# Optimization experiments

Measured on AMD Instinct MI355X. Metric: run time of the kernel, lower is better.

Reference implementation:

```python
import jax, jax.numpy as jnp
import numpy as np

B, C_IN, T, H, W = 4, 512, 4, 56, 56
G, GP, K = 8, 64, 56            # groups, group_planes, kernel_size (H == K)
OUT = G * GP                     # out_channels = 512
EPS = 1e-5


def setup_inputs() -> dict:
    key = jax.random.key(0)
    ks = jax.random.split(key, 9)
    x = jax.random.normal(ks[0], (B, C_IN, T, H, W), jnp.float32)
    w_qkv = jax.random.normal(ks[1], (2 * OUT, C_IN), jnp.float32) * np.sqrt(1.0 / C_IN)
    g_qkv = jax.random.uniform(ks[2], (2 * OUT,), jnp.float32, 0.5, 1.5)
    b_qkv = jax.random.normal(ks[3], (2 * OUT,), jnp.float32) * 0.1
    relative = jax.random.normal(ks[4], (2 * GP, 2 * K - 1), jnp.float32) * np.sqrt(1.0 / GP)
    g_sim = jax.random.uniform(ks[5], (3 * G,), jnp.float32, 0.5, 1.5)
    b_sim = jax.random.normal(ks[6], (3 * G,), jnp.float32) * 0.1
    g_out = jax.random.uniform(ks[7], (2 * OUT,), jnp.float32, 0.5, 1.5)
    b_out = jax.random.normal(ks[8], (2 * OUT,), jnp.float32) * 0.1
    return {"x": x, "w_qkv": w_qkv, "g_qkv": g_qkv, "b_qkv": b_qkv,
            "relative": relative, "g_sim": g_sim, "b_sim": b_sim,
            "g_out": g_out, "b_out": b_out}


def _bn(x, gamma, beta, axes):
    # training-mode batchnorm: batch stats over `axes`, per channel (dim 1)
    mean = jnp.mean(x, axes, keepdims=True)
    var = jnp.var(x, axes, keepdims=True)
    shp = [1] * x.ndim
    shp[1] = -1
    return gamma.reshape(shp) * (x - mean) * jax.lax.rsqrt(var + EPS) + beta.reshape(shp)


def reference(x, w_qkv, g_qkv, b_qkv, relative, g_sim, b_sim, g_out, b_out):
    # axial='height': (B,C,T,H,W) -> (B,T,W,C,H), attend along H
    xp = jnp.transpose(x, (0, 2, 4, 1, 3)).reshape(B * T * W, C_IN, H)
    # 1x1 Conv1d + BatchNorm1d
    qkv = _bn(jnp.einsum('oc,nch->noh', w_qkv, xp), g_qkv, b_qkv, (0, 2))
    qkv = qkv.reshape(-1, G, 2 * GP, H)
    q, k, v = qkv[:, :, :GP // 2], qkv[:, :, GP // 2:GP], qkv[:, :, GP:]
    qk = jnp.einsum('bgci,bgcj->bgij', q, k)
    # relative position embeddings gathered per (i, j) offset
    idx = jnp.arange(K)[:, None] - jnp.arange(K)[None, :] + K - 1  # (K, K)
    emb = relative[:, idx]                                         # (2*GP, K, K)
    q_e, k_e, v_e = emb[:GP // 2], emb[GP // 2:GP], emb[GP:]
    qr = jnp.einsum('bgci,cij->bgij', q, q_e)
    kr = jnp.swapaxes(jnp.einsum('bgci,cij->bgij', k, k_e), 2, 3)
    sim = _bn(jnp.concatenate([qk, qr, kr], axis=1), g_sim, b_sim, (0, 2, 3))
    sim = sim.reshape(-1, 3, G, H, H).sum(axis=1)
    sim = jax.nn.softmax(sim, axis=3)
    sv = jnp.einsum('bgij,bgcj->bgci', sim, v)
    sve = jnp.einsum('bgij,cij->bgci', sim, v_e)
    out = jnp.concatenate([sv, sve], axis=-1).reshape(-1, 2 * OUT, H)
    out = _bn(out, g_out, b_out, (0, 2))
    out = out.reshape(B, T, W, OUT, 2, H).sum(axis=-2)
    return jnp.transpose(out, (0, 3, 1, 4, 2))  # (B, OUT, T, H, W)
```

## Files before the change

### kernel.cpp

```cpp
#include <hip/hip_runtime.h>
#include <hip/hip_bf16.h>

#define EPS 1e-5f
typedef __hip_bfloat16 bf;
typedef __attribute__((ext_vector_type(8))) short bf16x8;
typedef __attribute__((ext_vector_type(4))) short s16x4;
typedef __attribute__((ext_vector_type(4))) float f32x4;

#define MFMA16(a, b, c) __builtin_amdgcn_mfma_f32_16x16x32_bf16(a, b, c, 0, 0, 0)

#define WS_QSUM     0
#define WS_QSQ      4096
#define WS_SIMSUM   8192
#define WS_SIMSQ    9728
#define WS_OUTSUM   11264
#define WS_OUTSQ    19456
#define WS_ZERO_END 27648
#define WS_AQKV     27648
#define WS_BQKV     28672
#define WS_ASIM     29696
#define WS_BSIM     29728
#define WS_AOUT     29760
#define WS_BOUT     30784

__device__ __forceinline__ void gload_lds16(const void* g, void* l) {
    __builtin_amdgcn_global_load_lds(
        (const __attribute__((address_space(1))) void*)g,
        (__attribute__((address_space(3))) void*)l, 16, 0, 0);
}
__device__ __forceinline__ float bfbits2f(short b) {
    return __uint_as_float(((uint32_t)(unsigned short)b) << 16);
}
__device__ __forceinline__ short f2bfbits(float f) {
    return (short)__hip_bfloat16_raw(__float2bfloat16(f)).x;
}

__global__ __launch_bounds__(256) void k0_transpose(const float* __restrict__ x,
                                                    bf* __restrict__ xbt) {
    int bid = blockIdx.x;
    int h = bid % 56, bt = bid / 56;
    int b = bt >> 2, t = bt & 3;
    __shared__ short tile[512 * 57];
    const float* src = x + (((size_t)(b * 512) * 4 + t) * 3136) + h * 56;
    for (int e = threadIdx.x; e < 512 * 56; e += 256) {
        int c = e / 56, w = e - c * 56;
        tile[c * 57 + w] = f2bfbits(src[(size_t)c * 12544 + w]);
    }
    __syncthreads();
    short* dst = reinterpret_cast<short*>(xbt);
    size_t pbase = ((size_t)bt * 56) * 56 + h;
    for (int e = threadIdx.x; e < 512 * 56; e += 256) {
        int w = e >> 9, c = e & 511;
        dst[(pbase + (size_t)w * 56) * 512 + c] = tile[c * 57 + w];
    }
}

__global__ __launch_bounds__(256) void kw_conv(const float* __restrict__ w, bf* __restrict__ wb) {
    int i = (blockIdx.x * 256 + threadIdx.x) * 4;
#pragma unroll
    for (int u = 0; u < 4; ++u) wb[i + u] = __float2bfloat16(w[i + u]);
}

__global__ __launch_bounds__(256) void kprep(const float* __restrict__ rel,
                                             short* __restrict__ relTq,
                                             short* __restrict__ relTk,
                                             short* __restrict__ relBv) {
    int tid = blockIdx.x * 256 + threadIdx.x;
    if (tid < 3584) {
        int d = tid >> 5, c = tid & 31;
        relTq[tid] = f2bfbits(d < 111 ? rel[c * 111 + d] : 0.f);
        relTk[tid] = f2bfbits(d < 111 ? rel[(32 + c) * 111 + d] : 0.f);
    } else if (tid < 11776) {
        int u = tid - 3584, c = u >> 7, d = u & 127;
        relBv[u] = f2bfbits(d < 111 ? rel[(64 + c) * 111 + d] : 0.f);
    }
}

__global__ __launch_bounds__(256) void k1_mfma(const bf* __restrict__ xbt,
                                               const bf* __restrict__ wb,
                                               short* __restrict__ qkP,
                                               short* __restrict__ vP,
                                               float* __restrict__ qsum,
                                               float* __restrict__ qsq) {
    __shared__ __align__(16) short As[8192];
    __shared__ __align__(16) short Bs[7168];
    int tid = threadIdx.x;
    int g  = blockIdx.x;
    int p0 = blockIdx.y * 112;
    int o0 = g * 128;
    const short* aG = reinterpret_cast<const short*>(wb);
    const short* bG = reinterpret_cast<const short*>(xbt);
    int wv = tid >> 6, l = tid & 63, r16 = l & 15, q4 = l >> 4;

    f32x4 acc[2][7];
#pragma unroll
    for (int i = 0; i < 2; ++i)
#pragma unroll
        for (int j = 0; j < 7; ++j) acc[i][j] = (f32x4){0.f, 0.f, 0.f, 0.f};

    int rowa0 = wv * 32 + r16, rowa1 = rowa0 + 16;

    for (int k0 = 0; k0 < 512; k0 += 64) {
        int ch = tid;
#pragma unroll
        for (int it = 0; it < 4; ++it, ch += 256) {
            int row = ch >> 3, c = ch & 7;
            int gc = (c ^ row) & 7;
            gload_lds16(aG + (((size_t)(o0 + row)) << 9) + k0 + gc * 8, &As[ch << 3]);
        }
        ch = tid;
#pragma unroll
        for (int it = 0; it < 3; ++it, ch += 256) {
            int row = ch >> 3, c = ch & 7;
            int gc = (c ^ row) & 7;
            gload_lds16(bG + (((size_t)(p0 + row)) << 9) + k0 + gc * 8, &Bs[ch << 3]);
        }
        if (tid < 128) {
            int u = tid + 768;
            int row = u >> 3, c = u & 7;
            int gc = (c ^ row) & 7;
            gload_lds16(bG + (((size_t)(p0 + row)) << 9) + k0 + gc * 8, &Bs[u << 3]);
        }
        __syncthreads();
#pragma unroll
        for (int kk = 0; kk < 2; ++kk) {
            int wch = kk * 4 + q4;
            bf16x8 a0 = *reinterpret_cast<const bf16x8*>(&As[rowa0 * 64 + ((wch ^ rowa0) & 7) * 8]);
            bf16x8 a1 = *reinterpret_cast<const bf16x8*>(&As[rowa1 * 64 + ((wch ^ rowa1) & 7) * 8]);
#pragma unroll
            for (int j = 0; j < 7; ++j) {
                int rowb = j * 16 + r16;
                bf16x8 bj = *reinterpret_cast<const bf16x8*>(&Bs[rowb * 64 + ((wch ^ rowb) & 7) * 8]);
                acc[0][j] = MFMA16(a0, bj, acc[0][j]);
                acc[1][j] = MFMA16(a1, bj, acc[1][j]);
            }
        }
        __syncthreads();
    }
    int bkt = blockIdx.y & 3;
#pragma unroll
    for (int i = 0; i < 2; ++i)
#pragma unroll
        for (int r = 0; r < 4; ++r) {
            float sA = 0.f, sB = 0.f;
#pragma unroll
            for (int j = 0; j < 7; ++j) { float v = acc[i][j][r]; sA += v; sB += v * v; }
#pragma unroll
            for (int mk = 1; mk < 16; mk <<= 1) { sA += __shfl_xor(sA, mk); sB += __shfl_xor(sB, mk); }
            if (r16 == 0) {
                int o = o0 + wv * 32 + i * 16 + q4 * 4 + r;
                atomicAdd(&qsum[o * 4 + bkt], sA);
                atomicAdd(&qsq [o * 4 + bkt], sB);
            }
        }
#pragma unroll
    for (int j = 0; j < 7; ++j) {
        int p = p0 + j * 16 + r16;
        size_t rowb = ((size_t)g * 50176 + p) * 64;
#pragma unroll
        for (int i = 0; i < 2; ++i) {
            int op = wv * 32 + i * 16 + q4 * 4;
            s16x4 pk;
#pragma unroll
            for (int r = 0; r < 4; ++r) pk[r] = f2bfbits(acc[i][j][r]);
            short* dst = (op < 64) ? (qkP + rowb + op) : (vP + rowb + (op - 64));
            *reinterpret_cast<s16x4*>(dst) = pk;
        }
    }
}

__global__ __launch_bounds__(256) void k1b_coef(const float* __restrict__ qsum, const float* __restrict__ qsq,
                                                const float* __restrict__ gamma, const float* __restrict__ beta,
                                                float* __restrict__ a_c, float* __restrict__ b_c) {
    int o = blockIdx.x * 256 + threadIdx.x;
    float s = qsum[o * 4] + qsum[o * 4 + 1] + qsum[o * 4 + 2] + qsum[o * 4 + 3];
    float s2 = qsq[o * 4] + qsq[o * 4 + 1] + qsq[o * 4 + 2] + qsq[o * 4 + 3];
    float inv = 1.f / 50176.f;
    float mean = s * inv;
    float var = s2 * inv - mean * mean;
    float a = gamma[o] * rsqrtf(var + EPS);
    a_c[o] = a; b_c[o] = beta[o] - a * mean;
}

__global__ __launch_bounds__(512) void kbn2(const short* __restrict__ qkP,
                                            short* __restrict__ vP,
                                            const float* __restrict__ aq, const float* __restrict__ bq,
                                            const short* __restrict__ relTq,
                                            const short* __restrict__ relTk,
                                            float* __restrict__ ssum, float* __restrict__ ssq) {
    __shared__ __align__(16) short qkTl[5120];
    __shared__ short vtl[64 * 57];
    __shared__ float red[48];
    int blk = blockIdx.x, n = blk >> 3, g = blk & 7, tid = threadIdx.x;
    size_t sb = ((size_t)g * 50176 + (size_t)n * 56) * 64;
    const short* qsrc = qkP + sb;
    short* vsrc = vP + sb;
    for (int u = tid; u < 448; u += 512) {
        int i = u >> 3, c0 = (u & 7) << 3;
        bf16x8 raw = *reinterpret_cast<const bf16x8*>(qsrc + i * 64 + c0);
        bf16x8 t;
#pragma unroll
        for (int uu = 0; uu < 8; ++uu) {
            int o = g * 128 + c0 + uu;
            t[uu] = f2bfbits(aq[o] * bfbits2f(raw[uu]) + bq[o]);
        }
        *reinterpret_cast<bf16x8*>(&qkTl[((c0 & 32) ? 2560 : 0) + i * 40 + (c0 & 31)]) = t;
    }
    for (int u = tid; u < 640; u += 512) {
        int part = u / 320, r = u - part * 320;
        qkTl[part * 2560 + (56 + r / 40) * 40 + (r % 40)] = 0;
    }
    for (int u = tid; u < 448; u += 512) {
        int i = u >> 3, c0 = (u & 7) << 3;
        bf16x8 raw = *reinterpret_cast<const bf16x8*>(vsrc + i * 64 + c0);
#pragma unroll
        for (int uu = 0; uu < 8; ++uu) {
            int o = g * 128 + 64 + c0 + uu;
            vtl[(c0 + uu) * 57 + i] = f2bfbits(aq[o] * bfbits2f(raw[uu]) + bq[o]);
        }
    }
    __syncthreads();
    for (int u = tid; u < 448; u += 512) {
        int c = u / 7, h0 = (u - c * 7) * 8;
        bf16x8 t;
#pragma unroll
        for (int uu = 0; uu < 8; ++uu) t[uu] = vtl[c * 57 + h0 + uu];
        *reinterpret_cast<bf16x8*>(vsrc + c * 56 + h0) = t;
    }
    int w = tid >> 6, l = tid & 63, m = w >> 1, s = w & 1, la = l & 15, lb = l >> 4;
    bf16x8 aqf = *reinterpret_cast<const bf16x8*>(&qkTl[(m * 16 + la) * 40 + lb * 8]);
    bf16x8 akf = *reinterpret_cast<const bf16x8*>(&qkTl[2560 + (m * 16 + la) * 40 + lb * 8]);
    float s0 = 0, s1 = 0, s2v = 0, q0 = 0, q1 = 0, q2 = 0;
#pragma unroll
    for (int t = 0; t < 2; ++t) {
        int nt = 2 * s + t;
        bf16x8 bk = *reinterpret_cast<const bf16x8*>(&qkTl[2560 + (nt * 16 + la) * 40 + lb * 8]);
        f32x4 acc = {0, 0, 0, 0};
        acc = MFMA16(aqf, bk, acc);
        int j = nt * 16 + la;
        if (j < 56) {
#pragma unroll
            for (int r = 0; r < 4; ++r) {
                int i = m * 16 + lb * 4 + r;
                if (i < 56) { float v = acc[r]; s0 += v; q0 += v * v; }
            }
        }
    }
    int ndt = s ? 3 : 4, dt0 = s * 4;
    for (int t = 0; t < ndt; ++t) {
        int dt = dt0 + t;
        bf16x8 br = *reinterpret_cast<const bf16x8*>(relTq + (dt * 16 + la) * 32 + lb * 8);
        f32x4 acc = {0, 0, 0, 0};
        acc = MFMA16(aqf, br, acc);
        int d = dt * 16 + la;
#pragma unroll
        for (int r = 0; r < 4; ++r) {
            int i = m * 16 + lb * 4 + r;
            if (i < 56 && d >= i && d <= i + 55) { float v = acc[r]; s1 += v; q1 += v * v; }
        }
    }
    for (int t = 0; t < ndt; ++t) {
        int dt = dt0 + t;
        bf16x8 br = *reinterpret_cast<const bf16x8*>(relTk + (dt * 16 + la) * 32 + lb * 8);
        f32x4 acc = {0, 0, 0, 0};
        acc = MFMA16(akf, br, acc);
        int d = dt * 16 + la;
#pragma unroll
        for (int r = 0; r < 4; ++r) {
            int j = m * 16 + lb * 4 + r;
            if (j < 56 && d >= j && d <= j + 55) { float v = acc[r]; s2v += v; q2 += v * v; }
        }
    }
    float vals[6] = {s0, s1, s2v, q0, q1, q2};
#pragma unroll
    for (int v = 0; v < 6; ++v) {
        for (int off = 32; off; off >>= 1) vals[v] += __shfl_down(vals[v], off);
        if (l == 0) red[v * 8 + w] = vals[v];
    }
    __syncthreads();
    if (tid < 6) {
        float tot = 0;
#pragma unroll
        for (int k = 0; k < 8; ++k) tot += red[tid * 8 + k];
        int comp = (tid < 3) ? tid : tid - 3;
        int ch = comp * 8 + g;
        int bkt = blk & 63;
        atomicAdd((tid < 3 ? ssum : ssq) + ch * 64 + bkt, tot);
    }
}

__global__ void k2b_coef(const float* __restrict__ ssum, const float* __restrict__ ssq,
                         const float* __restrict__ gs, const float* __restrict__ bs,
                         float* __restrict__ a_c, float* __restrict__ b_c) {
    int c = threadIdx.x;
    if (c >= 24) return;
    float s = 0, s2 = 0;
    for (int k = 0; k < 64; ++k) { s += ssum[c * 64 + k]; s2 += ssq[c * 64 + k]; }
    float inv = 1.f / 2809856.f;
    float mean = s * inv;
    float var = s2 * inv - mean * mean;
    float a = gs[c] * rsqrtf(var + EPS);
    a_c[c] = a; b_c[c] = bs[c] - a * mean;
}

__global__ __launch_bounds__(512, 6) void k3_mfma(const short* __restrict__ relTq,
                                                  const short* __restrict__ relTk,
                                                  const short* __restrict__ relBv,
                                                  short* __restrict__ qkP,
                                                  short* __restrict__ vP,
                                                  const float* __restrict__ aq, const float* __restrict__ bq,
                                                  const float* __restrict__ asim, const float* __restrict__ bsim,
                                                  float* __restrict__ osum, float* __restrict__ osq) {
    __shared__ __align__(16) char smem[51936];
    short* qkTl = (short*)smem;
    float* qkl  = (float*)(smem + 10240);
    short* Sql  = (short*)(smem + 23008);
    short* Krl  = (short*)(smem + 36448);
    short* simB = (short*)(smem + 23008);
    short* Pb   = (short*)(smem + 32224);
    short* vBl  = (short*)smem;
    float* red  = (float*)(smem + 49888);

    int blk = blockIdx.x, n = blk >> 3, g = blk & 7, tid = threadIdx.x;
    size_t sb = ((size_t)g * 50176 + (size_t)n * 56) * 64;
    short* svdst = qkP + sb;
    short* vHs   = vP + sb;

    bf16x8 vreg = {0, 0, 0, 0, 0, 0, 0, 0};
    int vc = tid / 7, vch = tid - vc * 7;
    if (tid < 448)
        vreg = *reinterpret_cast<const bf16x8*>(vHs + vc * 56 + vch * 8);

    for (int u = tid; u < 448; u += 512) {
        int i = u >> 3, c0 = (u & 7) << 3;
        bf16x8 raw = *reinterpret_cast<const bf16x8*>(svdst + i * 64 + c0);
        bf16x8 t;
#pragma unroll
        for (int uu = 0; uu < 8; ++uu) {
            int o = g * 128 + c0 + uu;
            t[uu] = f2bfbits(aq[o] * bfbits2f(raw[uu]) + bq[o]);
        }
        *reinterpret_cast<bf16x8*>(&qkTl[((c0 & 32) ? 2560 : 0) + i * 40 + (c0 & 31)]) = t;
    }
    for (int u = tid; u < 640; u += 512) {
        int part = u / 320, r = u - part * 320;
        qkTl[part * 2560 + (56 + r / 40) * 40 + (r % 40)] = 0;
    }
    __syncthreads();

    int w = tid >> 6, l = tid & 63, m = w >> 1, s = w & 1, la = l & 15, lb = l >> 4;
    int i0 = m * 16 + lb * 4;
    {
        bf16x8 aqf = *reinterpret_cast<const bf16x8*>(&qkTl[(m * 16 + la) * 40 + lb * 8]);
        bf16x8 akf = *reinterpret_cast<const bf16x8*>(&qkTl[(64 + m * 16 + la) * 40 + lb * 8]);
        __builtin_amdgcn_s_setprio(1);
#pragma unroll
        for (int t = 0; t < 2; ++t) {
            int nt = 2 * s + t;
            bf16x8 bk = *reinterpret_cast<const bf16x8*>(&qkTl[(64 + nt * 16 + la) * 40 + lb * 8]);
            f32x4 acc = {0, 0, 0, 0};
            acc = MFMA16(aqf, bk, acc);
            int j = nt * 16 + la;
            if (j < 56) {
#pragma unroll
                for (int r = 0; r < 4; ++r) {
                    int i = i0 + r;
                    if (i < 56) qkl[i * 57 + j] = acc[r];
                }
            }
        }
        int ndt = s ? 3 : 4, dt0 = s * 4;
        for (int t = 0; t < ndt; ++t) {
            int dt = dt0 + t;
            bf16x8 br = *reinterpret_cast<const bf16x8*>(relTq + (dt * 16 + la) * 32 + lb * 8);
            f32x4 acc = {0, 0, 0, 0};
            acc = MFMA16(aqf, br, acc);
            int d = dt * 16 + la;
            if (i0 < 56) {
                s16x4 pk;
#pragma unroll
                for (int r = 0; r < 4; ++r) pk[r] = f2bfbits(acc[r]);
                *reinterpret_cast<s16x4*>(&Sql[d * 60 + i0]) = pk;
            }
        }
        for (int t = 0; t < ndt; ++t) {
            int dt = dt0 + t;
            bf16x8 br = *reinterpret_cast<const bf16x8*>(relTk + (dt * 16 + la) * 32 + lb * 8);
            f32x4 acc = {0, 0, 0, 0};
            acc = MFMA16(akf, br, acc);
            int d = dt * 16 + la;
            if (i0 < 56) {
                s16x4 pk;
#pragma unroll
                for (int r = 0; r < 4; ++r) pk[r] = f2bfbits(acc[r]);
                *reinterpret_cast<s16x4*>(&Krl[d * 60 + i0]) = pk;
            }
        }
        __builtin_amdgcn_s_setprio(0);
    }
    __syncthreads();

    if (tid < 448)
        *reinterpret_cast<bf16x8*>(&vBl[vc * 72 + vch * 8]) = vreg;
    if (tid < 128) {
        int c = tid >> 1, chp = tid & 1;
        bf16x8 z = {0, 0, 0, 0, 0, 0, 0, 0};
        *reinterpret_cast<bf16x8*>(&vBl[c * 72 + 56 + chp * 8]) = z;
    }
    float a0 = asim[g], a1 = asim[8 + g], a2 = asim[16 + g];
    float bb = bsim[g] + bsim[8 + g] + bsim[16 + g];
    float p[7];
#pragma unroll
    for (int rr = 0; rr < 7; ++rr) {
        int i = w * 7 + rr;
        float sc = -1e30f;
        if (l < 56) {
            sc = a0 * qkl[i * 57 + l]
               + a1 * bfbits2f(Sql[(i - l + 55) * 60 + i])
               + a2 * bfbits2f(Krl[(l - i + 55) * 60 + l]) + bb;
        }
        float mx = sc;
#pragma unroll
        for (int off = 32; off; off >>= 1) mx = fmaxf(mx, __shfl_xor(mx, off));
        float e = (l < 56) ? __expf(sc - mx) : 0.f;
        float su = e;
#pragma unroll
        for (int off = 32; off; off >>= 1) su += __shfl_xor(su, off);
        p[rr] = e / su;
    }
    __syncthreads();

#pragma unroll
    for (int rr = 0; rr < 7; ++rr) {
        int i = w * 7 + rr;
        short pv = f2bfbits(p[rr]);
        simB[i * 72 + l] = (l < 56) ? pv : (short)0;
        if (l < 56) Pb[i * 136 + (i - l + 55)] = pv;
        if (l < i || l > i + 55) Pb[i * 136 + l] = 0;
        if (l > i - 9) Pb[i * 136 + l + 64] = 0;
        if (l < 8) Pb[i * 136 + l + 128] = 0;
    }
    __syncthreads();

    f32x4 sva[2]  = {{0, 0, 0, 0}, {0, 0, 0, 0}};
    f32x4 svea[2] = {{0, 0, 0, 0}, {0, 0, 0, 0}};
    __builtin_amdgcn_s_setprio(1);
#pragma unroll
    for (int ks = 0; ks < 2; ++ks) {
        bf16x8 av = *reinterpret_cast<const bf16x8*>(&vBl[(m * 16 + la) * 72 + ks * 32 + lb * 8]);
#pragma unroll
        for (int t = 0; t < 2; ++t) {
            int nt = 2 * s + t;
            bf16x8 bsf = *reinterpret_cast<const bf16x8*>(&simB[(nt * 16 + la) * 72 + ks * 32 + lb * 8]);
            sva[t] = MFMA16(av, bsf, sva[t]);
        }
    }
#pragma unroll
    for (int ks = 0; ks < 4; ++ks) {
        bf16x8 ar = *reinterpret_cast<const bf16x8*>(relBv + (m * 16 + la) * 128 + ks * 32 + lb * 8);
#pragma unroll
        for (int t = 0; t < 2; ++t) {
            int nt = 2 * s + t;
            bf16x8 bp = *reinterpret_cast<const bf16x8*>(&Pb[(nt * 16 + la) * 136 + ks * 32 + lb * 8]);
            svea[t] = MFMA16(ar, bp, svea[t]);
        }
    }
    __builtin_amdgcn_s_setprio(0);
    float st0[4] = {0, 0, 0, 0}, st1[4] = {0, 0, 0, 0}, st2[4] = {0, 0, 0, 0}, st3[4] = {0, 0, 0, 0};
#pragma unroll
    for (int t = 0; t < 2; ++t) {
        int i = (2 * s + t) * 16 + la;
        bool ok = i < 56;
#pragma unroll
        for (int r = 0; r < 4; ++r) {
            int c = m * 16 + lb * 4 + r;
            float va = sva[t][r], ve = svea[t][r];
            if (ok) {
                svdst[c * 56 + i] = f2bfbits(va);
                vHs  [c * 56 + i] = f2bfbits(ve);
                st0[r] += va; st1[r] += va * va; st2[r] += ve; st3[r] += ve * ve;
            }
        }
    }
#pragma unroll
    for (int r = 0; r < 4; ++r) {
#pragma unroll
        for (int mk = 1; mk < 16; mk <<= 1) {
            st0[r] += __shfl_xor(st0[r], mk);
            st1[r] += __shfl_xor(st1[r], mk);
            st2[r] += __shfl_xor(st2[r], mk);
            st3[r] += __shfl_xor(st3[r], mk);
        }
    }
    if (la == 0) {
#pragma unroll
        for (int r = 0; r < 4; ++r) {
            int c = m * 16 + lb * 4 + r;
            red[(0 * 64 + c) * 2 + s] = st0[r];
            red[(1 * 64 + c) * 2 + s] = st1[r];
            red[(2 * 64 + c) * 2 + s] = st2[r];
            red[(3 * 64 + c) * 2 + s] = st3[r];
        }
    }
    __syncthreads();
    if (tid < 64) {
        int c = tid, o2 = (g * 64 + c) * 2, bkt = blk & 7;
        atomicAdd(&osum[o2 * 8 + bkt],       red[(0 * 64 + c) * 2] + red[(0 * 64 + c) * 2 + 1]);
        atomicAdd(&osq [o2 * 8 + bkt],       red[(1 * 64 + c) * 2] + red[(1 * 64 + c) * 2 + 1]);
        atomicAdd(&osum[(o2 + 1) * 8 + bkt], red[(2 * 64 + c) * 2] + red[(2 * 64 + c) * 2 + 1]);
        atomicAdd(&osq [(o2 + 1) * 8 + bkt], red[(3 * 64 + c) * 2] + red[(3 * 64 + c) * 2 + 1]);
    }
}

__global__ __launch_bounds__(256) void k3b_coef(const float* __restrict__ osum, const float* __restrict__ osq,
                                                const float* __restrict__ go, const float* __restrict__ bo,
                                                float* __restrict__ a_c, float* __restrict__ b_c) {
    int o = blockIdx.x * 256 + threadIdx.x;
    float s = 0, s2 = 0;
#pragma unroll
    for (int k = 0; k < 8; ++k) { s += osum[o * 8 + k]; s2 += osq[o * 8 + k]; }
    float inv = 1.f / 50176.f;
    float mean = s * inv;
    float var = s2 * inv - mean * mean;
    float a = go[o] * rsqrtf(var + EPS);
    a_c[o] = a; b_c[o] = bo[o] - a * mean;
}

__global__ __launch_bounds__(256) void k4_out(const short* __restrict__ svq,
                                              const short* __restrict__ sve,
                                              const float* __restrict__ ao, const float* __restrict__ bo,
                                              float* __restrict__ out) {
    int blk = blockIdx.x;
    int oc = blk & 511, bt = blk >> 9;
    int b = bt >> 2, tt = bt & 3;
    int g = oc >> 6, c = oc & 63;
    __shared__ float tile[56][57];
    int tid = threadIdx.x;
    int o_sv = oc * 2, o_sve = oc * 2 + 1;
    float asv = ao[o_sv], bsv = bo[o_sv], asve = ao[o_sve], bsve = bo[o_sve];
    float badd = bsv + bsve;
    int nbase = (b * 4 + tt) * 56;
    for (int e = tid; e < 3136; e += 256) {
        int wq = e / 56, h = e - wq * 56;
        size_t idx = ((size_t)g * 50176 + (size_t)(nbase + wq) * 56) * 64 + c * 56 + h;
        tile[wq][h] = asv * bfbits2f(svq[idx]) + asve * bfbits2f(sve[idx]) + badd;
    }
    __syncthreads();
    size_t ob = ((size_t)(b * 512 + oc) * 4 + tt) * 3136;
    for (int e = tid; e < 3136; e += 256) {
        int h = e / 56, wq = e - h * 56;
        out[ob + h * 56 + wq] = tile[wq][h];
    }
}

extern "C" void kernel_launch(void* const* d_in, const int* in_sizes, int n_in,
                              void* d_out, int out_size, void* d_ws, size_t ws_size,
                              hipStream_t stream) {
    (void)in_sizes; (void)n_in; (void)out_size; (void)ws_size;
    const float* x     = (const float*)d_in[0];
    const float* w_qkv = (const float*)d_in[1];
    const float* g_qkv = (const float*)d_in[2];
    const float* b_qkv = (const float*)d_in[3];
    const float* rel   = (const float*)d_in[4];
    const float* g_sim = (const float*)d_in[5];
    const float* b_sim = (const float*)d_in[6];
    const float* g_out = (const float*)d_in[7];
    const float* b_out = (const float*)d_in[8];
    float* ws  = (float*)d_ws;
    float* out = (float*)d_out;
    short* qkP = (short*)((char*)d_ws + 131072);
    short* vP  = (short*)((char*)d_ws + 51511296);
    bf*    xbt = (bf*)d_out;
    bf*    wb  = (bf*)((char*)d_out + 51380224);
    short* relTq = (short*)((char*)d_out + 73400320);
    short* relTk = relTq + 3584;
    short* relBv = relTk + 3584;

    hipMemsetAsync(ws, 0, WS_ZERO_END * sizeof(float), stream);
    k0_transpose<<<896, 256, 0, stream>>>(x, xbt);
    kw_conv<<<512, 256, 0, stream>>>(w_qkv, wb);
    kprep<<<46, 256, 0, stream>>>(rel, relTq, relTk, relBv);
    k1_mfma<<<dim3(8, 448), 256, 0, stream>>>(xbt, wb, qkP, vP, ws + WS_QSUM, ws + WS_QSQ);
    k1b_coef<<<4, 256, 0, stream>>>(ws + WS_QSUM, ws + WS_QSQ, g_qkv, b_qkv,
                                    ws + WS_AQKV, ws + WS_BQKV);
    kbn2<<<7168, 512, 0, stream>>>(qkP, vP, ws + WS_AQKV, ws + WS_BQKV,
                                   relTq, relTk, ws + WS_SIMSUM, ws + WS_SIMSQ);
    k2b_coef<<<1, 64, 0, stream>>>(ws + WS_SIMSUM, ws + WS_SIMSQ, g_sim, b_sim,
                                   ws + WS_ASIM, ws + WS_BSIM);
    k3_mfma<<<7168, 512, 0, stream>>>(relTq, relTk, relBv, qkP, vP,
                                      ws + WS_AQKV, ws + WS_BQKV,
                                      ws + WS_ASIM, ws + WS_BSIM,
                                      ws + WS_OUTSUM, ws + WS_OUTSQ);
    k3b_coef<<<4, 256, 0, stream>>>(ws + WS_OUTSUM, ws + WS_OUTSQ, g_out, b_out,
                                    ws + WS_AOUT, ws + WS_BOUT);
    k4_out<<<8192, 256, 0, stream>>>(qkP, vP, ws + WS_AOUT, ws + WS_BOUT, out);
}
```

Before: 446.6 us.

## Accumulate scaled qk, qr, kr terms directly into shared sim buffer via LDS atomics

Instead of writing the relative-position MFMA results to separate bf16 Sql/Krl staging buffers and gathering them during softmax, each MFMA result is scaled by its batchnorm coefficient and atomically added into a single fp32 sim tile that is pre-initialised with the bias. This cuts LDS from about 52KB to 38KB, so more blocks can fit per CU, and it drops the gather and bf16 round-trip. In exchange it adds many LDS float atomics with contention and removes the occupancy hint from launch bounds. An extra barrier is added before the reduction buffer is written, since red now overlaps regions still in use.

Measured after the change: 751.5 us. +68.3%, slower.

```diff
diff --git a/kernel.cpp b/kernel.cpp
--- a/kernel.cpp
+++ b/kernel.cpp
@@ -303,29 +303,30 @@
     a_c[c] = a; b_c[c] = bs[c] - a * mean;
 }
 
-__global__ __launch_bounds__(512, 6) void k3_mfma(const short* __restrict__ relTq,
-                                                  const short* __restrict__ relTk,
-                                                  const short* __restrict__ relBv,
-                                                  short* __restrict__ qkP,
-                                                  short* __restrict__ vP,
-                                                  const float* __restrict__ aq, const float* __restrict__ bq,
-                                                  const float* __restrict__ asim, const float* __restrict__ bsim,
-                                                  float* __restrict__ osum, float* __restrict__ osq) {
-    __shared__ __align__(16) char smem[51936];
+__global__ __launch_bounds__(512) void k3_mfma(const short* __restrict__ relTq,
+                                               const short* __restrict__ relTk,
+                                               const short* __restrict__ relBv,
+                                               short* __restrict__ qkP,
+                                               short* __restrict__ vP,
+                                               const float* __restrict__ aq, const float* __restrict__ bq,
+                                               const float* __restrict__ asim, const float* __restrict__ bsim,
+                                               float* __restrict__ osum, float* __restrict__ osq) {
+    __shared__ __align__(16) char smem[38912];
     short* qkTl = (short*)smem;
     float* qkl  = (float*)(smem + 10240);
-    short* Sql  = (short*)(smem + 23008);
-    short* Krl  = (short*)(smem + 36448);
-    short* simB = (short*)(smem + 23008);
-    short* Pb   = (short*)(smem + 32224);
+    short* simB = (short*)(smem + 10240);
+    short* Pb   = (short*)(smem + 19456);
     short* vBl  = (short*)smem;
-    float* red  = (float*)(smem + 49888);
+    float* red  = (float*)(smem + 36864);
 
     int blk = blockIdx.x, n = blk >> 3, g = blk & 7, tid = threadIdx.x;
     size_t sb = ((size_t)g * 50176 + (size_t)n * 56) * 64;
     short* svdst = qkP + sb;
     short* vHs   = vP + sb;
 
+    float a0 = asim[g], a1 = asim[8 + g], a2 = asim[16 + g];
+    float bb = bsim[g] + bsim[8 + g] + bsim[16 + g];
+
     bf16x8 vreg = {0, 0, 0, 0, 0, 0, 0, 0};
     int vc = tid / 7, vch = tid - vc * 7;
     if (tid < 448)
@@ -346,6 +347,7 @@
         int part = u / 320, r = u - part * 320;
         qkTl[part * 2560 + (56 + r / 40) * 40 + (r % 40)] = 0;
     }
+    for (int e = tid; e < 3192; e += 512) qkl[e] = bb;
     __syncthreads();
 
     int w = tid >> 6, l = tid & 63, m = w >> 1, s = w & 1, la = l & 15, lb = l >> 4;
@@ -365,7 +367,7 @@
 #pragma unroll
                 for (int r = 0; r < 4; ++r) {
                     int i = i0 + r;
-                    if (i < 56) qkl[i * 57 + j] = acc[r];
+                    if (i < 56) atomicAdd(&qkl[i * 57 + j], a0 * acc[r]);
                 }
             }
         }
@@ -376,11 +378,11 @@
             f32x4 acc = {0, 0, 0, 0};
             acc = MFMA16(aqf, br, acc);
             int d = dt * 16 + la;
-            if (i0 < 56) {
-                s16x4 pk;
-#pragma unroll
-                for (int r = 0; r < 4; ++r) pk[r] = f2bfbits(acc[r]);
-                *reinterpret_cast<s16x4*>(&Sql[d * 60 + i0]) = pk;
+#pragma unroll
+            for (int r = 0; r < 4; ++r) {
+                int i = i0 + r;
+                if (i < 56 && d >= i && d <= i + 55)
+                    atomicAdd(&qkl[i * 57 + (i - d + 55)], a1 * acc[r]);
             }
         }
         for (int t = 0; t < ndt; ++t) {
@@ -389,11 +391,11 @@
             f32x4 acc = {0, 0, 0, 0};
             acc = MFMA16(akf, br, acc);
             int d = dt * 16 + la;
-            if (i0 < 56) {
-                s16x4 pk;
-#pragma unroll
-                for (int r = 0; r < 4; ++r) pk[r] = f2bfbits(acc[r]);
-                *reinterpret_cast<s16x4*>(&Krl[d * 60 + i0]) = pk;
+#pragma unroll
+            for (int r = 0; r < 4; ++r) {
+                int jj = i0 + r;
+                if (jj < 56 && d >= jj && d <= jj + 55)
+                    atomicAdd(&qkl[(jj - d + 55) * 57 + jj], a2 * acc[r]);
             }
         }
         __builtin_amdgcn_s_setprio(0);
@@ -407,18 +409,11 @@
         bf16x8 z = {0, 0, 0, 0, 0, 0, 0, 0};
         *reinterpret_cast<bf16x8*>(&vBl[c * 72 + 56 + chp * 8]) = z;
     }
-    float a0 = asim[g], a1 = asim[8 + g], a2 = asim[16 + g];
-    float bb = bsim[g] + bsim[8 + g] + bsim[16 + g];
     float p[7];
 #pragma unroll
     for (int rr = 0; rr < 7; ++rr) {
         int i = w * 7 + rr;
-        float sc = -1e30f;
-        if (l < 56) {
-            sc = a0 * qkl[i * 57 + l]
-               + a1 * bfbits2f(Sql[(i - l + 55) * 60 + i])
-               + a2 * bfbits2f(Krl[(l - i + 55) * 60 + l]) + bb;
-        }
+        float sc = (l < 56) ? qkl[i * 57 + l] : -1e30f;
         float mx = sc;
 #pragma unroll
         for (int off = 32; off; off >>= 1) mx = fmaxf(mx, __shfl_xor(mx, off));
@@ -492,6 +487,7 @@
             st3[r] += __shfl_xor(st3[r], mk);
         }
     }
+    __syncthreads();
     if (la == 0) {
 #pragma unroll
         for (int r = 0; r < 4; ++r) {
```
